# Optimization experiments

Measured on AMD Instinct MI355X. Metric: run time of the kernel, lower is better.

Reference implementation:

```python
import jax, jax.numpy as jnp
import numpy as np

N_GENES = 978

def setup_inputs() -> dict:
    key = jax.random.key(0)
    ks = jax.random.split(key, 8)
    B = 8192
    N = B * N_GENES  # 8,009,856 nodes
    E = 20_000_000
    inputs = jax.random.normal(ks[0], (B, N_GENES), dtype=jnp.float32)
    edges = jax.random.randint(ks[1], (2, E), 0, N, dtype=jnp.int64)
    gcn_w = jax.random.normal(ks[2], (1, 1), dtype=jnp.float32)
    gcn_b = jax.random.normal(ks[3], (1,), dtype=jnp.float32)
    W1 = jax.random.normal(ks[4], (N_GENES, 2048), dtype=jnp.float32) * 0.03
    b1 = jax.random.normal(ks[5], (2048,), dtype=jnp.float32) * 0.01
    W2 = jax.random.normal(ks[6], (2048, 100), dtype=jnp.float32) * 0.02
    b2 = jax.random.normal(ks[7], (100,), dtype=jnp.float32) * 0.01
    return {"inputs": inputs, "edges": edges, "gcn_w": gcn_w, "gcn_b": gcn_b,
            "W1": W1, "b1": b1, "W2": W2, "b2": b2}

def reference(inputs, edges, gcn_w, gcn_b, W1, b1, W2, b2):
    B = inputs.shape[0]
    N = B * N_GENES
    # GCNConv(1,1, add_self_loops=False, normalize=False):
    # x' = x * w; out[dst] = sum over edges of x'[src]; out += bias
    x = inputs.reshape(-1) * gcn_w[0, 0]            # [N] node scalars
    src, dst = edges[0], edges[1]                   # messages flow src -> dst
    agg = jax.ops.segment_sum(x[src], dst, num_segments=N)  # irregular scatter-add
    agg = agg + gcn_b[0]
    h = agg.reshape(B, N_GENES)
    h = jax.nn.relu(h)                              # dropout = identity (eval)
    h = jax.nn.relu(h @ W1 + b1)                    # [B, 2048]
    out = h @ W2 + b2                               # [B, 100]
    return out
```

## Files before the change

### kernel.cpp

```cpp
#include <hip/hip_runtime.h>
#include <hip/hip_bf16.h>
#include <stdint.h>


typedef unsigned short u16;
typedef unsigned int u32;
typedef __bf16 bf16x8 __attribute__((ext_vector_type(8)));
typedef float f32x4 __attribute__((ext_vector_type(4)));

#define NGENES 978
#define KPAD   1024
#define H1DIM  2048
#define NOUT   100
#define NOUTP  112
#define KSPLIT 8

#define NB      978
#define BSH     13
#define BNODES  8192
#define SC_WGS  256
#define SC_THR  1024
#define SDEPTH  32
#define OVFCAP  256
#define CAP_B   24576

__device__ __forceinline__ u16 f2b(float f) {
    unsigned u = __builtin_bit_cast(unsigned, f);
    u = (u + 0x7FFFu + ((u >> 16) & 1u)) >> 16;
    return (u16)u;
}

__device__ __forceinline__ u32 nt_u32(const u32* p) {
    return __builtin_nontemporal_load(p);
}
__device__ __forceinline__ float nt_f32(const float* p) {
    return __builtin_nontemporal_load(p);
}

__device__ __forceinline__ void gl2lds16(const void* g, void* l) {
    __builtin_amdgcn_global_load_lds(
        (const __attribute__((address_space(1))) void*)(uintptr_t)g,
        (__attribute__((address_space(3))) void*)(unsigned)(uintptr_t)l,
        16, 0, 0);
}

__global__ void detect_kernel(const unsigned* __restrict__ e, int* __restrict__ flag) {
    if (threadIdx.x == 0) {
        int is64 = 1;
        for (int i = 0; i < 64; ++i) {
            if (e[2 * i + 1] != 0u) { is64 = 0; break; }
        }
        *flag = is64;
    }
}

__global__ void xbf_kernel(const float* __restrict__ x, const float* __restrict__ gcn_w,
                           u16* __restrict__ xb, int N) {
    const float w = gcn_w[0];
    int i = (blockIdx.x * 256 + threadIdx.x) * 4;
    if (i + 3 < N) {
        float4 v = *(const float4*)&x[i];
        xb[i + 0] = f2b(v.x * w);
        xb[i + 1] = f2b(v.y * w);
        xb[i + 2] = f2b(v.z * w);
        xb[i + 3] = f2b(v.w * w);
    } else {
        for (int k = i; k < N; ++k) xb[k] = f2b(x[k] * w);
    }
}

__global__ __launch_bounds__(SC_THR) void binscatter_kernel(const void* __restrict__ edges,
                                                            const u16* __restrict__ xb,
                                                            const int* __restrict__ flag, int E,
                                                            u32* __restrict__ pairs,
                                                            u32* __restrict__ cnt,
                                                            u32* __restrict__ ovfg,
                                                            u32* __restrict__ ovfcnt) {
    __shared__ u32 sfill[NB];
    __shared__ u32 stage[SDEPTH * NB];
    __shared__ u32 ovf[OVFCAP * 2];
    __shared__ u32 ocount;
    const int tid = threadIdx.x;
    for (int b = tid; b < NB; b += SC_THR) sfill[b] = 0;
    if (tid == 0) ocount = 0;
    __syncthreads();

    const int per = (E + SC_WGS - 1) / SC_WGS;
    const int s = blockIdx.x * per;
    const int e = min(E, s + per);
    const u32* eb = (const u32*)edges;
    const int st = (*flag) ? 2 : 1;
    const u32* sp = eb;
    const u32* dp = eb + (size_t)st * E;

    for (int base_i = s; base_i < e; base_i += 8 * SC_THR) {
        const int idx = base_i + tid;
        u32 srcv[8], dv[8];
        u16 val[8];
#pragma unroll
        for (int k = 0; k < 8; ++k) {
            int i = idx + k * SC_THR;
            bool ok = i < e;
            srcv[k] = ok ? nt_u32(&sp[(size_t)st * i]) : 0u;
            dv[k]   = ok ? nt_u32(&dp[(size_t)st * i]) : 0xFFFFFFFFu;
        }
#pragma unroll
        for (int k = 0; k < 8; ++k)
            val[k] = (dv[k] != 0xFFFFFFFFu) ? xb[srcv[k]] : (u16)0;

#pragma unroll
        for (int h = 0; h < 2; ++h) {
#pragma unroll
            for (int k = 4 * h; k < 4 * h + 4; ++k) {
                if (dv[k] != 0xFFFFFFFFu) {
                    u32 b = dv[k] >> BSH;
                    u32 pr = ((dv[k] & (BNODES - 1)) << 16) | (u32)val[k];
                    u32 slot = atomicAdd(&sfill[b], 1u);
                    if (slot < SDEPTH) {
                        stage[slot * NB + b] = pr;
                    } else {
                        atomicSub(&sfill[b], 1u);
                        u32 o = atomicAdd(&ocount, 1u);
                        if (o < OVFCAP) {
                            ovf[o * 2] = b; ovf[o * 2 + 1] = pr;
                        } else {
                            u32 og = atomicAdd(ovfcnt, 1u);
                            ovfg[og * 2] = (b << BSH) | (pr >> 16);
                            ovfg[og * 2 + 1] = pr & 0xFFFFu;
                        }
                    }
                }
            }
            __syncthreads();
            for (int b = tid; b < NB; b += SC_THR) {
                u32 f = sfill[b];
                u32 nl = f >> 4;
                if (nl) {
                    u32 base = atomicAdd(&cnt[b], nl << 4);
                    for (u32 g = 0; g < nl; ++g) {
                        u32 wb = base + (g << 4);
                        if (wb < CAP_B) {
                            u32* dst = &pairs[(size_t)b * CAP_B + wb];
#pragma unroll
                            for (int q = 0; q < 4; ++q) {
                                uint4 v;
                                v.x = stage[(g * 16 + q * 4 + 0) * NB + b];
                                v.y = stage[(g * 16 + q * 4 + 1) * NB + b];
                                v.z = stage[(g * 16 + q * 4 + 2) * NB + b];
                                v.w = stage[(g * 16 + q * 4 + 3) * NB + b];
                                *(uint4*)&dst[q * 4] = v;
                            }
                        } else {
                            for (int q = 0; q < 16; ++q) {
                                u32 pr = stage[(g * 16 + q) * NB + b];
                                u32 og = atomicAdd(ovfcnt, 1u);
                                ovfg[og * 2] = (b << BSH) | (pr >> 16);
                                ovfg[og * 2 + 1] = pr & 0xFFFFu;
                            }
                        }
                    }
                    u32 n16 = nl << 4;
                    u32 rem = f & 15u;
                    for (u32 r = 0; r < rem; ++r)
                        stage[r * NB + b] = stage[(n16 + r) * NB + b];
                    sfill[b] = rem;
                }
            }
            __syncthreads();
            u32 oc = ocount;
            if (oc) {
                u32 m = oc < (u32)OVFCAP ? oc : (u32)OVFCAP;
                if (tid < (int)m) {
                    u32 b = ovf[tid * 2];
                    u32 pr = ovf[tid * 2 + 1];
                    u32 slot = atomicAdd(&sfill[b], 1u);
                    if (slot < SDEPTH) {
                        stage[slot * NB + b] = pr;
                    } else {
                        atomicSub(&sfill[b], 1u);
                        u32 og = atomicAdd(ovfcnt, 1u);
                        ovfg[og * 2] = (b << BSH) | (pr >> 16);
                        ovfg[og * 2 + 1] = pr & 0xFFFFu;
                    }
                }
                __syncthreads();
                if (tid == 0) ocount = 0;
                __syncthreads();
            }
        }
    }
    for (int b = tid; b < NB; b += SC_THR) {
        u32 f = sfill[b];
        if (f) {
            u32 padded = (f + 15u) & ~15u;
            u32 base = atomicAdd(&cnt[b], padded);
            for (u32 g = 0; g < (padded >> 4); ++g) {
                u32 wb = base + (g << 4);
                if (wb < CAP_B) {
                    u32* dst = &pairs[(size_t)b * CAP_B + wb];
#pragma unroll
                    for (int q = 0; q < 4; ++q) {
                        uint4 v;
                        u32 j = g * 16 + q * 4;
                        v.x = (j + 0 < f) ? stage[(j + 0) * NB + b] : 0u;
                        v.y = (j + 1 < f) ? stage[(j + 1) * NB + b] : 0u;
                        v.z = (j + 2 < f) ? stage[(j + 2) * NB + b] : 0u;
                        v.w = (j + 3 < f) ? stage[(j + 3) * NB + b] : 0u;
                        *(uint4*)&dst[q * 4] = v;
                    }
                } else {
                    for (u32 q = g * 16; q < f && q < g * 16 + 16; ++q) {
                        u32 pr = stage[q * NB + b];
                        u32 og = atomicAdd(ovfcnt, 1u);
                        ovfg[og * 2] = (b << BSH) | (pr >> 16);
                        ovfg[og * 2 + 1] = pr & 0xFFFFu;
                    }
                }
            }
        }
    }
}

__global__ __launch_bounds__(512) void accum_kernel(const u32* __restrict__ pairs,
                                                    const u32* __restrict__ cnt,
                                                    float* __restrict__ agg) {
    __shared__ float acc[BNODES];
    for (int i = threadIdx.x; i < BNODES; i += 512) acc[i] = 0.f;
    __syncthreads();
    const int b = blockIdx.x;
    u32 n = cnt[b];
    if (n > CAP_B) n = CAP_B;
    const u32 p0 = (u32)b * CAP_B;
    const u32 p1 = p0 + n;
    u32 p = p0 + threadIdx.x;
    for (; p + 3 * 512 < p1; p += 4 * 512) {
        u32 pk[4];
#pragma unroll
        for (int k = 0; k < 4; ++k) pk[k] = nt_u32(&pairs[p + k * 512]);
#pragma unroll
        for (int k = 0; k < 4; ++k) {
            if (pk[k]) {
                float v = __builtin_bit_cast(float, (pk[k] & 0xFFFFu) << 16);
                atomicAdd(&acc[pk[k] >> 16], v);
            }
        }
    }
    for (; p < p1; p += 512) {
        u32 pk = nt_u32(&pairs[p]);
        if (pk) {
            float v = __builtin_bit_cast(float, (pk & 0xFFFFu) << 16);
            atomicAdd(&acc[pk >> 16], v);
        }
    }
    __syncthreads();
    const size_t node0 = (size_t)b << BSH;
    for (int i = threadIdx.x; i < BNODES; i += 512) agg[node0 + i] = acc[i];
}

__global__ void ovf_fix_kernel(const u32* __restrict__ ovfg, const u32* __restrict__ ovfcnt,
                               float* __restrict__ agg) {
    u32 n = *ovfcnt;
    for (u32 i = blockIdx.x * 256 + threadIdx.x; i < n; i += gridDim.x * 256) {
        float v = __builtin_bit_cast(float, ovfg[i * 2 + 1] << 16);
        atomicAdd(&agg[ovfg[i * 2]], v);
    }
}

__global__ void scatter_kernel(const void* __restrict__ edges, const float* __restrict__ x,
                               const float* __restrict__ gcn_w, float* __restrict__ agg,
                               const int* __restrict__ flag, int E) {
    long long e = (long long)blockIdx.x * 256 + threadIdx.x;
    if (e >= E) return;
    int s, d;
    if (*flag) {
        const long long* e64 = (const long long*)edges;
        s = (int)e64[e];
        d = (int)e64[(long long)E + e];
    } else {
        const int* e32 = (const int*)edges;
        s = e32[e];
        d = e32[(long long)E + e];
    }
    atomicAdd(&agg[d], x[s] * gcn_w[0]);
}

__global__ void act_kernel(const float* __restrict__ agg, const float* __restrict__ gcn_b,
                           u16* __restrict__ A) {
    int idx = blockIdx.x * 256 + threadIdx.x;
    int i = idx >> 10;
    int k = idx & 1023;
    float v = 0.f;
    if (k < NGENES) {
        v = nt_f32(&agg[(size_t)i * NGENES + k]) + gcn_b[0];
        v = v > 0.f ? v : 0.f;
    }
    A[idx] = f2b(v);
}

__global__ void transposeW1(const float* __restrict__ W1, u16* __restrict__ W1T) {
    __shared__ float t[32][33];
    int n0 = blockIdx.x * 32;
    int k0 = blockIdx.y * 32;
    int tx = threadIdx.x, ty = threadIdx.y;
    for (int r = ty; r < 32; r += 8) {
        int k = k0 + r;
        t[r][tx] = (k < NGENES) ? W1[(size_t)k * H1DIM + n0 + tx] : 0.f;
    }
    __syncthreads();
    for (int r = ty; r < 32; r += 8) {
        int n = n0 + r;
        W1T[(size_t)n * KPAD + k0 + tx] = f2b(t[tx][r]);
    }
}

__global__ void transposeW2(const float* __restrict__ W2, u16* __restrict__ W2T) {
    __shared__ float t[32][33];
    int n0 = blockIdx.x * 32;
    int k0 = blockIdx.y * 32;
    int tx = threadIdx.x, ty = threadIdx.y;
    for (int r = ty; r < 32; r += 8) {
        int k = k0 + r;
        int n = n0 + tx;
        t[r][tx] = (n < NOUT) ? W2[(size_t)k * NOUT + n] : 0.f;
    }
    __syncthreads();
    for (int r = ty; r < 32; r += 8) {
        int n = n0 + r;
        if (n < NOUTP) W2T[(size_t)n * H1DIM + k0 + tx] = f2b(t[tx][r]);
    }
}

__global__ __launch_bounds__(256) void gemm1_kernel(const u16* __restrict__ A,
                                                    const u16* __restrict__ Bt,
                                                    const float* __restrict__ b1,
                                                    u16* __restrict__ H) {
    __shared__ u16 As[128 * 32];
    __shared__ u16 Bs[128 * 32];
    const int tid = threadIdx.x;
    const int m0 = blockIdx.y * 128;
    const int n0 = blockIdx.x * 128;
    const int wave = tid >> 6;
    const int lane = tid & 63;
    const int wm = (wave >> 1) * 64;
    const int wn = (wave & 1) * 64;
    const int quad = lane >> 4;
    const int l16 = lane & 15;

    f32x4 acc[4][4];
#pragma unroll
    for (int i = 0; i < 4; ++i)
#pragma unroll
        for (int j = 0; j < 4; ++j)
            acc[i][j] = (f32x4){0.f, 0.f, 0.f, 0.f};

    const int ch0 = tid, ch1 = tid + 256;
    const u16* ag0 = A + (size_t)(m0 + (ch0 >> 2)) * KPAD + (ch0 & 3) * 8;
    const u16* ag1 = A + (size_t)(m0 + (ch1 >> 2)) * KPAD + (ch1 & 3) * 8;
    const u16* bg0 = Bt + (size_t)(n0 + (ch0 >> 2)) * KPAD + (ch0 & 3) * 8;
    const u16* bg1 = Bt + (size_t)(n0 + (ch1 >> 2)) * KPAD + (ch1 & 3) * 8;
    u16* la0 = &As[ch0 * 8];
    u16* la1 = &As[ch1 * 8];
    u16* lb0 = &Bs[ch0 * 8];
    u16* lb1 = &Bs[ch1 * 8];

    for (int k0 = 0; k0 < KPAD; k0 += 32) {
        gl2lds16(ag0, la0);
        gl2lds16(ag1, la1);
        gl2lds16(bg0, lb0);
        gl2lds16(bg1, lb1);
        ag0 += 32; ag1 += 32; bg0 += 32; bg1 += 32;
        __syncthreads();

        bf16x8 af[4], bfr[4];
#pragma unroll
        for (int i = 0; i < 4; ++i)
            af[i] = *(const bf16x8*)&As[(wm + i * 16 + l16) * 32 + quad * 8];
#pragma unroll
        for (int j = 0; j < 4; ++j)
            bfr[j] = *(const bf16x8*)&Bs[(wn + j * 16 + l16) * 32 + quad * 8];
#pragma unroll
        for (int i = 0; i < 4; ++i)
#pragma unroll
            for (int j = 0; j < 4; ++j)
                acc[i][j] = __builtin_amdgcn_mfma_f32_16x16x32_bf16(af[i], bfr[j], acc[i][j], 0, 0, 0);
        __syncthreads();
    }

#pragma unroll
    for (int j = 0; j < 4; ++j) {
        const int col = n0 + wn + j * 16 + l16;
        const float bv = b1[col];
#pragma unroll
        for (int i = 0; i < 4; ++i) {
            const int rbase = m0 + wm + i * 16 + quad * 4;
#pragma unroll
            for (int r = 0; r < 4; ++r) {
                float v = acc[i][j][r] + bv;
                v = v > 0.f ? v : 0.f;
                H[(size_t)(rbase + r) * H1DIM + col] = f2b(v);
            }
        }
    }
}

__global__ __launch_bounds__(256) void gemm2_kernel(const u16* __restrict__ Hh,
                                                    const u16* __restrict__ W2T,
                                                    const float* __restrict__ b2,
                                                    float* __restrict__ out) {
    __shared__ u16 As[64 * 32];
    __shared__ u16 Bs[NOUTP * 32];
    const int tid = threadIdx.x;
    const int m0 = blockIdx.y * 64;
    const int kc = blockIdx.x;
    const int kbase = kc * (H1DIM / KSPLIT);
    const int wave = tid >> 6;
    const int lane = tid & 63;
    const int quad = lane >> 4;
    const int l16 = lane & 15;

    f32x4 acc[7];
#pragma unroll
    for (int j = 0; j < 7; ++j) acc[j] = (f32x4){0.f, 0.f, 0.f, 0.f};

    const u16* ag = Hh + (size_t)(m0 + (tid >> 2)) * H1DIM + kbase + (tid & 3) * 8;
    u16* la = &As[tid * 8];
    const u16* bg0 = W2T + (size_t)(tid >> 2) * H1DIM + kbase + (tid & 3) * 8;
    u16* lb0 = &Bs[tid * 8];
    const int ch1 = tid + 256;
    const u16* bg1 = W2T + (size_t)(ch1 >> 2) * H1DIM + kbase + (ch1 & 3) * 8;
    u16* lb1 = &Bs[ch1 * 8];
    const bool bact = (ch1 < NOUTP * 4);

    for (int kk = 0; kk < H1DIM / KSPLIT; kk += 32) {
        gl2lds16(ag, la);
        gl2lds16(bg0, lb0);
        if (bact) gl2lds16(bg1, lb1);
        ag += 32; bg0 += 32; bg1 += 32;
        __syncthreads();

        bf16x8 af = *(const bf16x8*)&As[(wave * 16 + l16) * 32 + quad * 8];
#pragma unroll
        for (int j = 0; j < 7; ++j) {
            bf16x8 bfr = *(const bf16x8*)&Bs[(j * 16 + l16) * 32 + quad * 8];
            acc[j] = __builtin_amdgcn_mfma_f32_16x16x32_bf16(af, bfr, acc[j], 0, 0, 0);
        }
        __syncthreads();
    }

#pragma unroll
    for (int j = 0; j < 7; ++j) {
        const int col = j * 16 + l16;
        if (col < NOUT) {
            const float bv = (kc == 0) ? b2[col] : 0.f;
            const int rbase = m0 + wave * 16 + quad * 4;
#pragma unroll
            for (int r = 0; r < 4; ++r)
                atomicAdd(&out[(size_t)(rbase + r) * NOUT + col], acc[j][r] + bv);
        }
    }
}

extern "C" void kernel_launch(void* const* d_in, const int* in_sizes, int n_in,
                              void* d_out, int out_size, void* d_ws, size_t ws_size,
                              hipStream_t stream) {
    const float* inputs = (const float*)d_in[0];
    const void*  edges  = d_in[1];
    const float* gcn_w  = (const float*)d_in[2];
    const float* gcn_b  = (const float*)d_in[3];
    const float* W1     = (const float*)d_in[4];
    const float* b1     = (const float*)d_in[5];
    const float* W2     = (const float*)d_in[6];
    const float* b2     = (const float*)d_in[7];
    float* out = (float*)d_out;

    const int N = in_sizes[0];
    const int Brows = N / NGENES;
    const int E = in_sizes[1] / 2;

    char* ws = (char*)d_ws;
    size_t off = 0;
    auto carve = [&](size_t bytes) -> void* {
        void* p = ws + off;
        off = (off + bytes + 255) & ~(size_t)255;
        return p;
    };
    float* agg = (float*)carve((size_t)N * 4);
    u16*   Abf = (u16*)carve((size_t)Brows * KPAD * 2);
    u16*   W1T = (u16*)carve((size_t)H1DIM * KPAD * 2);
    u16*   W2Tp = (u16*)carve((size_t)NOUTP * H1DIM * 2);
    u16*   H1  = (u16*)carve((size_t)Brows * H1DIM * 2);
    int*   flag = (int*)carve(256);
    u16*   xb     = (u16*)carve((size_t)N * 2);
    u32*   cnt    = (u32*)carve((size_t)(NB + 64) * 4);
    u32*   ovfcnt = cnt + NB;
    u32*   ovfg   = (u32*)carve((size_t)(1 << 20) * 8);
    u32*   pairs  = (u32*)carve((size_t)NB * CAP_B * 4);
    const bool use_binned = (off <= ws_size);

    hipMemsetAsync(out, 0, (size_t)out_size * 4, stream);
    detect_kernel<<<1, 64, 0, stream>>>((const unsigned*)edges, flag);

    if (use_binned) {
        hipMemsetAsync(cnt, 0, (size_t)(NB + 64) * 4, stream);
        xbf_kernel<<<(N / 4 + 255) / 256, 256, 0, stream>>>(inputs, gcn_w, xb, N);
        binscatter_kernel<<<SC_WGS, SC_THR, 0, stream>>>(edges, xb, flag, E,
                                                         pairs, cnt, ovfg, ovfcnt);
        accum_kernel<<<NB, 512, 0, stream>>>(pairs, cnt, agg);
        ovf_fix_kernel<<<8, 256, 0, stream>>>(ovfg, ovfcnt, agg);
    } else {
        hipMemsetAsync(agg, 0, (size_t)N * 4, stream);
        const int sblocks = (E + 255) / 256;
        scatter_kernel<<<sblocks, 256, 0, stream>>>(edges, inputs, gcn_w, agg, flag, E);
    }

    act_kernel<<<(Brows * KPAD) / 256, 256, 0, stream>>>(agg, gcn_b, Abf);

    transposeW1<<<dim3(H1DIM / 32, KPAD / 32), dim3(32, 8), 0, stream>>>(W1, W1T);
    transposeW2<<<dim3(4, H1DIM / 32), dim3(32, 8), 0, stream>>>(W2, W2Tp);

    gemm1_kernel<<<dim3(H1DIM / 128, Brows / 128), 256, 0, stream>>>(Abf, W1T, b1, H1);
    gemm2_kernel<<<dim3(KSPLIT, Brows / 64), 256, 0, stream>>>(H1, W2Tp, b2, out);
}
```

Measured before the change: 786.3 us.

## Pre-bin edges by source octant so the xb gather stays cache-resident

Adds a first binning pass that splits edges into 8 buckets by source-node range of 1M nodes each. Each bucket stores a packed (dst, local src) 64-bit entry in a workspace buffer that is aliased with the later GEMM buffers. Each binscatter workgroup then processes one bucket, so its random reads of the bf16 node values touch only a 2MB slice instead of the whole array. This is meant to improve cache hit rates on the irregular gather. The cost is an extra full read and write pass over the edge list and a new overflow fix-up kernel; the in-LDS overflow staging is removed and streaming stores become nontemporal.

Measured after the change: 874.5 us. +11.2%, slower.

```diff
diff --git a/kernel.cpp b/kernel.cpp
--- a/kernel.cpp
+++ b/kernel.cpp
@@ -5,8 +5,10 @@
 
 typedef unsigned short u16;
 typedef unsigned int u32;
+typedef unsigned long long u64;
 typedef __bf16 bf16x8 __attribute__((ext_vector_type(8)));
 typedef float f32x4 __attribute__((ext_vector_type(4)));
+typedef unsigned int u32x4 __attribute__((ext_vector_type(4)));
 
 #define NGENES 978
 #define KPAD   1024
@@ -21,8 +23,15 @@
 #define SC_WGS  256
 #define SC_THR  1024
 #define SDEPTH  32
-#define OVFCAP  256
 #define CAP_B   24576
+
+#define NOCT     8
+#define OCT_SH   20
+#define OCT_NODES (1u << 20)
+#define RSTRIDE  2686976u
+#define ODEPTH   512
+#define NWG_A    2048
+#define A_THR    256
 
 __device__ __forceinline__ u16 f2b(float f) {
     unsigned u = __builtin_bit_cast(unsigned, f);
@@ -35,6 +44,9 @@
 }
 __device__ __forceinline__ float nt_f32(const float* p) {
     return __builtin_nontemporal_load(p);
+}
+__device__ __forceinline__ void nt_store4(u32x4 v, u32* p) {
+    __builtin_nontemporal_store(v, (u32x4*)p);
 }
 
 __device__ __forceinline__ void gl2lds16(const void* g, void* l) {
@@ -69,71 +81,171 @@
     }
 }
 
-__global__ __launch_bounds__(SC_THR) void binscatter_kernel(const void* __restrict__ edges,
+__global__ __launch_bounds__(A_THR) void binoct_kernel(const void* __restrict__ edges,
+                                                       const int* __restrict__ flag, int E,
+                                                       u64* __restrict__ ebuf,
+                                                       u32* __restrict__ ocnt,
+                                                       u64* __restrict__ ovfe,
+                                                       u32* __restrict__ ovfecnt) {
+    __shared__ u64 stA[NOCT][ODEPTH];
+    __shared__ u32 ofill[NOCT];
+    __shared__ u32 gbase[NOCT], gn[NOCT];
+    const int tid = threadIdx.x;
+    if (tid < NOCT) ofill[tid] = 0;
+    __syncthreads();
+
+    const int per = (E + NWG_A - 1) / NWG_A;
+    const int s = blockIdx.x * per;
+    const int e = min(E, s + per);
+    const u32* eb = (const u32*)edges;
+    const int st = (*flag) ? 2 : 1;
+    const u32* sp = eb;
+    const u32* dp = eb + (size_t)st * E;
+
+    for (int base_i = s; base_i < e; base_i += 8 * A_THR) {
+        u32 sv[8], dv[8];
+#pragma unroll
+        for (int k = 0; k < 8; ++k) {
+            int i = base_i + tid + k * A_THR;
+            bool ok = i < e;
+            sv[k] = ok ? nt_u32(&sp[(size_t)st * i]) : 0xFFFFFFFFu;
+            dv[k] = ok ? nt_u32(&dp[(size_t)st * i]) : 0u;
+        }
+#pragma unroll
+        for (int k = 0; k < 8; ++k) {
+            if (sv[k] != 0xFFFFFFFFu) {
+                u32 o = sv[k] >> OCT_SH;
+                u64 ent = ((u64)dv[k] << OCT_SH) | (u64)(sv[k] & (OCT_NODES - 1));
+                u32 slot = atomicAdd(&ofill[o], 1u);
+                if (slot < ODEPTH) {
+                    stA[o][slot] = ent;
+                } else {
+                    u32 og = atomicAdd(ovfecnt, 1u);
+                    ovfe[og] = ((u64)dv[k] << 32) | (u64)sv[k];
+                }
+            }
+        }
+        __syncthreads();
+        if (tid < NOCT) {
+            u32 f = min(ofill[tid], (u32)ODEPTH);
+            u32 nl = f >> 3;
+            gn[tid] = nl;
+            gbase[tid] = nl ? atomicAdd(&ocnt[tid], nl << 3) : 0u;
+        }
+        __syncthreads();
+        {
+            const int b = tid >> 5;
+            const u32 g0 = tid & 31;
+            for (u32 g = g0; g < gn[b]; g += 32) {
+                u32 base = gbase[b] + (g << 3);
+                if (base < RSTRIDE) {
+                    u64* dst = &ebuf[(size_t)b * RSTRIDE + base];
+#pragma unroll
+                    for (int q = 0; q < 4; ++q) {
+                        u64 w0 = stA[b][g * 8 + q * 2];
+                        u64 w1 = stA[b][g * 8 + q * 2 + 1];
+                        u32x4 v;
+                        v.x = (u32)w0; v.y = (u32)(w0 >> 32);
+                        v.z = (u32)w1; v.w = (u32)(w1 >> 32);
+                        nt_store4(v, (u32*)&dst[q * 2]);
+                    }
+                } else {
+                    for (int q = 0; q < 8; ++q) {
+                        u64 ent = stA[b][g * 8 + q];
+                        u32 d = (u32)(ent >> OCT_SH);
+                        u32 srcg = ((u32)b << OCT_SH) | ((u32)ent & (OCT_NODES - 1));
+                        u32 og = atomicAdd(ovfecnt, 1u);
+                        ovfe[og] = ((u64)d << 32) | (u64)srcg;
+                    }
+                }
+            }
+        }
+        __syncthreads();
+        if (tid < NOCT) {
+            u32 f = min(ofill[tid], (u32)ODEPTH);
+            u32 n8 = gn[tid] << 3;
+            for (u32 r = n8; r < f; ++r) stA[tid][r - n8] = stA[tid][r];
+            ofill[tid] = f - n8;
+        }
+        __syncthreads();
+    }
+    if (tid < NOCT) {
+        u32 f = min(ofill[tid], (u32)ODEPTH);
+        if (f) {
+            u32 base = atomicAdd(&ocnt[tid], 8u);
+            if (base < RSTRIDE) {
+                u64* dst = &ebuf[(size_t)tid * RSTRIDE + base];
+                for (u32 q = 0; q < 8; ++q)
+                    dst[q] = (q < f) ? stA[tid][q] : ~0ull;
+            } else {
+                for (u32 q = 0; q < f; ++q) {
+                    u64 ent = stA[tid][q];
+                    u32 d = (u32)(ent >> OCT_SH);
+                    u32 srcg = ((u32)tid << OCT_SH) | ((u32)ent & (OCT_NODES - 1));
+                    u32 og = atomicAdd(ovfecnt, 1u);
+                    ovfe[og] = ((u64)d << 32) | (u64)srcg;
+                }
+            }
+        }
+    }
+}
+
+__global__ __launch_bounds__(SC_THR) void binscatter_kernel(const u64* __restrict__ ebuf,
+                                                            const u32* __restrict__ ocnt,
                                                             const u16* __restrict__ xb,
-                                                            const int* __restrict__ flag, int E,
                                                             u32* __restrict__ pairs,
                                                             u32* __restrict__ cnt,
                                                             u32* __restrict__ ovfg,
                                                             u32* __restrict__ ovfcnt) {
     __shared__ u32 sfill[NB];
     __shared__ u32 stage[SDEPTH * NB];
-    __shared__ u32 ovf[OVFCAP * 2];
-    __shared__ u32 ocount;
     const int tid = threadIdx.x;
     for (int b = tid; b < NB; b += SC_THR) sfill[b] = 0;
-    if (tid == 0) ocount = 0;
     __syncthreads();
 
-    const int per = (E + SC_WGS - 1) / SC_WGS;
-    const int s = blockIdx.x * per;
-    const int e = min(E, s + per);
-    const u32* eb = (const u32*)edges;
-    const int st = (*flag) ? 2 : 1;
-    const u32* sp = eb;
-    const u32* dp = eb + (size_t)st * E;
-
-    for (int base_i = s; base_i < e; base_i += 8 * SC_THR) {
-        const int idx = base_i + tid;
-        u32 srcv[8], dv[8];
+    const int o = blockIdx.x & 7;
+    const int sub = blockIdx.x >> 3;
+    u32 n = ocnt[o]; if (n > RSTRIDE) n = RSTRIDE;
+    const u64* eo = ebuf + (size_t)o * RSTRIDE;
+    const u16* xbo = xb + ((size_t)o << OCT_SH);
+    const u32 per = (n + 31) / 32;
+    const u32 s = sub * per;
+    const u32 e = min(n, s + per);
+
+    for (u32 base_i = s; base_i < e; base_i += 8 * SC_THR) {
+        u64 ev[8];
+#pragma unroll
+        for (int k = 0; k < 8; ++k) {
+            u32 i = base_i + tid + k * SC_THR;
+            ev[k] = (i < e) ? __builtin_nontemporal_load(&eo[i]) : ~0ull;
+        }
+        u32 d[8];
         u16 val[8];
 #pragma unroll
         for (int k = 0; k < 8; ++k) {
-            int i = idx + k * SC_THR;
-            bool ok = i < e;
-            srcv[k] = ok ? nt_u32(&sp[(size_t)st * i]) : 0u;
-            dv[k]   = ok ? nt_u32(&dp[(size_t)st * i]) : 0xFFFFFFFFu;
-        }
-#pragma unroll
-        for (int k = 0; k < 8; ++k)
-            val[k] = (dv[k] != 0xFFFFFFFFu) ? xb[srcv[k]] : (u16)0;
-
+            d[k] = (u32)(ev[k] >> OCT_SH);
+            val[k] = (ev[k] != ~0ull) ? xbo[(u32)ev[k] & (OCT_NODES - 1)] : (u16)0;
+        }
 #pragma unroll
         for (int h = 0; h < 2; ++h) {
 #pragma unroll
             for (int k = 4 * h; k < 4 * h + 4; ++k) {
-                if (dv[k] != 0xFFFFFFFFu) {
-                    u32 b = dv[k] >> BSH;
-                    u32 pr = ((dv[k] & (BNODES - 1)) << 16) | (u32)val[k];
+                if (ev[k] != ~0ull) {
+                    u32 b = d[k] >> BSH;
+                    u32 pr = ((d[k] & (BNODES - 1)) << 16) | (u32)val[k];
                     u32 slot = atomicAdd(&sfill[b], 1u);
                     if (slot < SDEPTH) {
                         stage[slot * NB + b] = pr;
                     } else {
-                        atomicSub(&sfill[b], 1u);
-                        u32 o = atomicAdd(&ocount, 1u);
-                        if (o < OVFCAP) {
-                            ovf[o * 2] = b; ovf[o * 2 + 1] = pr;
-                        } else {
-                            u32 og = atomicAdd(ovfcnt, 1u);
-                            ovfg[og * 2] = (b << BSH) | (pr >> 16);
-                            ovfg[og * 2 + 1] = pr & 0xFFFFu;
-                        }
+                        u32 og = atomicAdd(ovfcnt, 1u);
+                        ovfg[og * 2] = d[k];
+                        ovfg[og * 2 + 1] = pr & 0xFFFFu;
                     }
                 }
             }
             __syncthreads();
             for (int b = tid; b < NB; b += SC_THR) {
-                u32 f = sfill[b];
+                u32 f = min(sfill[b], (u32)SDEPTH);
                 u32 nl = f >> 4;
                 if (nl) {
                     u32 base = atomicAdd(&cnt[b], nl << 4);
@@ -143,54 +255,36 @@
                             u32* dst = &pairs[(size_t)b * CAP_B + wb];
 #pragma unroll
                             for (int q = 0; q < 4; ++q) {
-                                uint4 v;
+                                u32x4 v;
                                 v.x = stage[(g * 16 + q * 4 + 0) * NB + b];
                                 v.y = stage[(g * 16 + q * 4 + 1) * NB + b];
                                 v.z = stage[(g * 16 + q * 4 + 2) * NB + b];
                                 v.w = stage[(g * 16 + q * 4 + 3) * NB + b];
-                                *(uint4*)&dst[q * 4] = v;
+                                nt_store4(v, &dst[q * 4]);
                             }
                         } else {
                             for (int q = 0; q < 16; ++q) {
                                 u32 pr = stage[(g * 16 + q) * NB + b];
                                 u32 og = atomicAdd(ovfcnt, 1u);
-                                ovfg[og * 2] = (b << BSH) | (pr >> 16);
+                                ovfg[og * 2] = ((u32)b << BSH) | (pr >> 16);
                                 ovfg[og * 2 + 1] = pr & 0xFFFFu;
                             }
                         }
                     }
                     u32 n16 = nl << 4;
-                    u32 rem = f & 15u;
+                    u32 rem = f - n16;
                     for (u32 r = 0; r < rem; ++r)
                         stage[r * NB + b] = stage[(n16 + r) * NB + b];
                     sfill[b] = rem;
+                } else {
+                    sfill[b] = f;
                 }
             }
             __syncthreads();
-            u32 oc = ocount;
-            if (oc) {
-                u32 m = oc < (u32)OVFCAP ? oc : (u32)OVFCAP;
-                if (tid < (int)m) {
-                    u32 b = ovf[tid * 2];
-                    u32 pr = ovf[tid * 2 + 1];
-                    u32 slot = atomicAdd(&sfill[b], 1u);
-                    if (slot < SDEPTH) {
-                        stage[slot * NB + b] = pr;
-                    } else {
-                        atomicSub(&sfill[b], 1u);
-                        u32 og = atomicAdd(ovfcnt, 1u);
-                        ovfg[og * 2] = (b << BSH) | (pr >> 16);
-                        ovfg[og * 2 + 1] = pr & 0xFFFFu;
-                    }
-                }
-                __syncthreads();
-                if (tid == 0) ocount = 0;
-                __syncthreads();
-            }
         }
     }
     for (int b = tid; b < NB; b += SC_THR) {
-        u32 f = sfill[b];
+        u32 f = min(sfill[b], (u32)SDEPTH);
         if (f) {
             u32 padded = (f + 15u) & ~15u;
             u32 base = atomicAdd(&cnt[b], padded);
@@ -200,19 +294,19 @@
                     u32* dst = &pairs[(size_t)b * CAP_B + wb];
 #pragma unroll
                     for (int q = 0; q < 4; ++q) {
-                        uint4 v;
+                        u32x4 v;
                         u32 j = g * 16 + q * 4;
                         v.x = (j + 0 < f) ? stage[(j + 0) * NB + b] : 0u;
                         v.y = (j + 1 < f) ? stage[(j + 1) * NB + b] : 0u;
                         v.z = (j + 2 < f) ? stage[(j + 2) * NB + b] : 0u;
                         v.w = (j + 3 < f) ? stage[(j + 3) * NB + b] : 0u;
-                        *(uint4*)&dst[q * 4] = v;
+                        nt_store4(v, &dst[q * 4]);
                     }
                 } else {
                     for (u32 q = g * 16; q < f && q < g * 16 + 16; ++q) {
                         u32 pr = stage[q * NB + b];
                         u32 og = atomicAdd(ovfcnt, 1u);
-                        ovfg[og * 2] = (b << BSH) | (pr >> 16);
+                        ovfg[og * 2] = ((u32)b << BSH) | (pr >> 16);
                         ovfg[og * 2 + 1] = pr & 0xFFFFu;
                     }
                 }
@@ -263,6 +357,18 @@
     for (u32 i = blockIdx.x * 256 + threadIdx.x; i < n; i += gridDim.x * 256) {
         float v = __builtin_bit_cast(float, ovfg[i * 2 + 1] << 16);
         atomicAdd(&agg[ovfg[i * 2]], v);
+    }
+}
+
+__global__ void ovfe_fix_kernel(const u64* __restrict__ ovfe, const u32* __restrict__ ovfecnt,
+                                const u16* __restrict__ xb, float* __restrict__ agg) {
+    u32 n = *ovfecnt;
+    for (u32 i = blockIdx.x * 256 + threadIdx.x; i < n; i += gridDim.x * 256) {
+        u64 ev = ovfe[i];
+        u32 srcg = (u32)ev;
+        u32 d = (u32)(ev >> 32);
+        float v = __builtin_bit_cast(float, ((u32)xb[srcg]) << 16);
+        atomicAdd(&agg[d], v);
     }
 }
 
@@ -484,18 +590,30 @@
         off = (off + bytes + 255) & ~(size_t)255;
         return p;
     };
-    float* agg = (float*)carve((size_t)N * 4);
-    u16*   Abf = (u16*)carve((size_t)Brows * KPAD * 2);
-    u16*   W1T = (u16*)carve((size_t)H1DIM * KPAD * 2);
-    u16*   W2Tp = (u16*)carve((size_t)NOUTP * H1DIM * 2);
-    u16*   H1  = (u16*)carve((size_t)Brows * H1DIM * 2);
+    u64* ebuf = (u64*)carve((size_t)NOCT * RSTRIDE * 8);
+    char* ali = (char*)ebuf;
+    auto aliascarve = [&](size_t bytes) -> void* {
+        void* p = ali;
+        ali += (bytes + 255) & ~(size_t)255;
+        return p;
+    };
+    float* agg  = (float*)aliascarve((size_t)N * 4);
+    u16*   Abf  = (u16*)aliascarve((size_t)Brows * KPAD * 2);
+    u16*   W1T  = (u16*)aliascarve((size_t)H1DIM * KPAD * 2);
+    u16*   W2Tp = (u16*)aliascarve((size_t)NOUTP * H1DIM * 2);
+    u16*   H1   = (u16*)aliascarve((size_t)Brows * H1DIM * 2);
+
     int*   flag = (int*)carve(256);
-    u16*   xb     = (u16*)carve((size_t)N * 2);
-    u32*   cnt    = (u32*)carve((size_t)(NB + 64) * 4);
-    u32*   ovfcnt = cnt + NB;
-    u32*   ovfg   = (u32*)carve((size_t)(1 << 20) * 8);
-    u32*   pairs  = (u32*)carve((size_t)NB * CAP_B * 4);
-    const bool use_binned = (off <= ws_size);
+    u16*   xb   = (u16*)carve((size_t)N * 2);
+    u32*   cnt  = (u32*)carve((size_t)(NB + 64) * 4);
+    u32*   ocnt    = cnt + NB;
+    u32*   ovfcnt  = cnt + NB + 8;
+    u32*   ovfecnt = cnt + NB + 9;
+    u32*   ovfg = (u32*)carve((size_t)(1 << 19) * 8);
+    u64*   ovfe = (u64*)carve((size_t)(1 << 18) * 8);
+    u32*   pairs = (u32*)carve((size_t)NB * CAP_B * 4);
+    const bool use_binned = (off <= ws_size) && (N <= (NOCT << OCT_SH)) &&
+                            ((char*)ali <= (char*)ebuf + (size_t)NOCT * RSTRIDE * 8);
 
     hipMemsetAsync(out, 0, (size_t)out_size * 4, stream);
     detect_kernel<<<1, 64, 0, stream>>>((const unsigned*)edges, flag);
@@ -503,10 +621,13 @@
     if (use_binned) {
         hipMemsetAsync(cnt, 0, (size_t)(NB + 64) * 4, stream);
         xbf_kernel<<<(N / 4 + 255) / 256, 256, 0, stream>>>(inputs, gcn_w, xb, N);
-        binscatter_kernel<<<SC_WGS, SC_THR, 0, stream>>>(edges, xb, flag, E,
+        binoct_kernel<<<NWG_A, A_THR, 0, stream>>>(edges, flag, E, ebuf, ocnt,
+                                                   ovfe, ovfecnt);
+        binscatter_kernel<<<SC_WGS, SC_THR, 0, stream>>>(ebuf, ocnt, xb,
                                                          pairs, cnt, ovfg, ovfcnt);
         accum_kernel<<<NB, 512, 0, stream>>>(pairs, cnt, agg);
         ovf_fix_kernel<<<8, 256, 0, stream>>>(ovfg, ovfcnt, agg);
+        ovfe_fix_kernel<<<8, 256, 0, stream>>>(ovfe, ovfecnt, xb, agg);
     } else {
         hipMemsetAsync(agg, 0, (size_t)N * 4, stream);
         const int sblocks = (E + 255) / 256;
```
